# Kernel optimization log

Hardware: AMD Instinct MI355X
Metric: run time of the kernel (lower is better)

The kernel has to match this reference:

```python
import jax, jax.numpy as jnp
import numpy as np

N_NODES = 50000
N_EDGES = 800000
N_GRAPHS = 256
D_IN, D_H1, D_H2, D_OUT = 64, 64, 64, 64


def gcn_conv(x, W, b, src, dst, n_nodes):
    # PyG GCNConv (eval): h = x @ W; add self-loops; deg[i] = in_deg(i) + 1;
    # out[i] = sum_{j->i} h[j] * deg[i]^-1/2 deg[j]^-1/2 + h[i]/deg[i] + b
    h = x @ W  # [N, F]
    ones = jnp.ones((src.shape[0],), dtype=x.dtype)
    deg = jax.ops.segment_sum(ones, dst, num_segments=n_nodes) + 1.0  # self loop
    dinv = jax.lax.rsqrt(deg)
    norm = dinv[src] * dinv[dst]  # [E]
    msg = h[src] * norm[:, None]  # [E, F]  (memory-bound gather)
    agg = jax.ops.segment_sum(msg, dst, num_segments=n_nodes)  # scatter-add
    agg = agg + h * (1.0 / deg)[:, None]  # self-loop contribution
    return agg + b


def setup_inputs() -> dict:
    key = jax.random.key(0)
    ks = jax.random.split(key, 12)
    x = jax.random.normal(ks[0], (N_NODES, D_IN), dtype=jnp.float32)
    src = jax.random.randint(ks[1], (N_EDGES,), 0, N_NODES)
    dst = jax.random.randint(ks[2], (N_EDGES,), 0, N_NODES)
    batch = jnp.sort(jax.random.randint(ks[3], (N_NODES,), 0, N_GRAPHS))
    def glorot(k, fin, fout):
        s = jnp.sqrt(6.0 / (fin + fout))
        return jax.random.uniform(k, (fin, fout), jnp.float32, -s, s)
    return {
        "x": x, "src": src, "dst": dst, "batch": batch,
        "W1": glorot(ks[4], D_IN, D_H1), "b1": jnp.zeros((D_H1,), jnp.float32),
        "W2": glorot(ks[5], D_H1, D_H2), "b2": jnp.zeros((D_H2,), jnp.float32),
        "W3": glorot(ks[6], D_H2, D_OUT), "b3": jnp.zeros((D_OUT,), jnp.float32),
        "Wl": glorot(ks[7], D_OUT, 1), "bl": jnp.zeros((1,), jnp.float32),
    }


def reference(x, src, dst, batch, W1, b1, W2, b2, W3, b3, Wl, bl):
    n = x.shape[0]
    h = jax.nn.relu(gcn_conv(x, W1, b1, src, dst, n))   # dropout inactive (eval)
    h = jax.nn.relu(gcn_conv(h, W2, b2, src, dst, n))
    h = jax.nn.relu(gcn_conv(h, W3, b3, src, dst, n))
    # global_mean_pool over graph ids
    sums = jax.ops.segment_sum(h, batch, num_segments=N_GRAPHS)  # [G, F]
    cnt = jax.ops.segment_sum(jnp.ones((n,), h.dtype), batch, num_segments=N_GRAPHS)
    pooled = sums / jnp.maximum(cnt, 1.0)[:, None]
    return pooled @ Wl + bl  # [G, 1]
```

## Files before the change

kernel.cpp:

```cpp
#include <hip/hip_runtime.h>

#define N_NODES 50000
#define N_EDGES 800000
#define N_GRAPHS 256
#define F 64
#define NBUCK 196
#define CAP 4608
#define P3_TILE 2048
#define P3_GRID ((N_EDGES + P3_TILE - 1) / P3_TILE)
#define BCAP 6144

__device__ __forceinline__ unsigned short f2bf(float f) {
    union { float f; unsigned u; } c; c.f = f;
    unsigned u = c.u + 0x7FFFu + ((c.u >> 16) & 1u);
    return (unsigned short)(u >> 16);
}
__device__ __forceinline__ unsigned pack2bf(float lo, float hi) {
    return (unsigned)f2bf(lo) | ((unsigned)f2bf(hi) << 16);
}
__device__ __forceinline__ float bfl(unsigned u) {
    union { unsigned u; float f; } c; c.u = u << 16; return c.f;
}
__device__ __forceinline__ float bfh(unsigned u) {
    union { unsigned u; float f; } c; c.u = u & 0xFFFF0000u; return c.f;
}

__global__ __launch_bounds__(256) void partition_edges(const int* __restrict__ src,
                                                       const int* __restrict__ dst,
                                                       int* __restrict__ bcur,
                                                       unsigned int* __restrict__ bpair) {
    __shared__ int bh[NBUCK], bloc[NBUCK], bpos[NBUCK];
    int t = threadIdx.x;
    int lo = blockIdx.x * P3_TILE;
    int hi = min(lo + P3_TILE, N_EDGES);
    for (int i = t; i < NBUCK; i += 256) { bh[i] = 0; bpos[i] = 0; }
    __syncthreads();
    for (int e = lo + t; e < hi; e += 256) atomicAdd(&bh[dst[e] >> 8], 1);
    __syncthreads();
    for (int i = t; i < NBUCK; i += 256)
        bloc[i] = bh[i] ? atomicAdd(&bcur[i], bh[i]) : 0;
    __syncthreads();
    for (int e = lo + t; e < hi; e += 256) {
        int d = dst[e];
        int b = d >> 8;
        int r = atomicAdd(&bpos[b], 1);
        bpair[(size_t)b * CAP + bloc[b] + r] = ((unsigned)src[e] << 8) | (unsigned)(d & 255);
    }
}

__global__ __launch_bounds__(256) void bucket_sort(const unsigned int* __restrict__ bpair,
                                                   const int* __restrict__ bcur,
                                                   int* __restrict__ eidx,
                                                   int* __restrict__ rbeg,
                                                   int* __restrict__ rend,
                                                   float* __restrict__ dinv) {
    __shared__ int cnt[256], s[256], pos[256];
    __shared__ int lout[BCAP];
    int b = blockIdx.x, t = threadIdx.x;
    int base = b * CAP;
    int sz = bcur[b];

    cnt[t] = 0;
    __syncthreads();
    for (int i = t; i < sz; i += 256) atomicAdd(&cnt[bpair[base + i] & 255], 1);
    __syncthreads();
    int v = cnt[t];
    s[t] = v;
    __syncthreads();
    for (int off = 1; off < 256; off <<= 1) {
        int u = (t >= off) ? s[t - off] : 0;
        __syncthreads();
        s[t] += u;
        __syncthreads();
    }
    int excl = s[t] - v;
    pos[t] = excl;
    int node = b * 256 + t;
    if (node < N_NODES) {
        rbeg[node] = base + excl;
        rend[node] = base + excl + v;
        dinv[node] = 1.0f / sqrtf((float)v + 1.0f);
    }
    __syncthreads();

    if (sz <= BCAP) {
        for (int i = t; i < sz; i += 256) {
            unsigned p = bpair[base + i];
            int r = atomicAdd(&pos[p & 255], 1);
            lout[r] = (int)((p >> 8) << 7);
        }
        __syncthreads();
        for (int i = t; i < sz; i += 256) eidx[base + i] = lout[i];
    } else {
        for (int i = t; i < sz; i += 256) {
            unsigned p = bpair[base + i];
            int r = atomicAdd(&pos[p & 255], 1);
            eidx[base + r] = (int)((p >> 8) << 7);
        }
    }
}

#define XSTRIDE 17
template <bool BF16IN>
__global__ __launch_bounds__(256) void gemm64_t(const void* __restrict__ Xv,
                                                const float* __restrict__ W,
                                                const float* __restrict__ dinv,
                                                unsigned short* __restrict__ Hn, int n) {
    __shared__ float4 sW[64 * 16];
    __shared__ float4 sX[128 * XSTRIDE];
    int tid = threadIdx.x;
    int base = blockIdx.x * 128;

    const float4* W4 = (const float4*)W;
    for (int i = tid; i < 64 * 16; i += 256) sW[i] = W4[i];
    if (BF16IN) {
        const uint4* X4 = (const uint4*)Xv;
        for (int i = tid; i < 128 * 8; i += 256) {
            int r = i >> 3, c = i & 7;
            int node = base + r;
            uint4 u = (node < n) ? X4[(size_t)node * 8 + c]
                                 : make_uint4(0u, 0u, 0u, 0u);
            sX[r * XSTRIDE + 2 * c]     = make_float4(bfl(u.x), bfh(u.x), bfl(u.y), bfh(u.y));
            sX[r * XSTRIDE + 2 * c + 1] = make_float4(bfl(u.z), bfh(u.z), bfl(u.w), bfh(u.w));
        }
    } else {
        const float4* X4 = (const float4*)Xv;
        for (int i = tid; i < 128 * 16; i += 256) {
            int r = i >> 4, kg = i & 15;
            int node = base + r;
            sX[r * XSTRIDE + kg] = (node < n) ? X4[(size_t)node * 16 + kg]
                                              : make_float4(0.f, 0.f, 0.f, 0.f);
        }
    }
    __syncthreads();

    int fg = tid & 15;
    int ng = tid >> 4;
    float4 acc[8];
#pragma unroll
    for (int ii = 0; ii < 8; ii++) acc[ii] = make_float4(0.f, 0.f, 0.f, 0.f);

    for (int kg = 0; kg < 16; kg++) {
        float4 xv[8];
#pragma unroll
        for (int ii = 0; ii < 8; ii++) xv[ii] = sX[(ng + 16 * ii) * XSTRIDE + kg];
#pragma unroll
        for (int kk = 0; kk < 4; kk++) {
            float4 wv = sW[(4 * kg + kk) * 16 + fg];
#pragma unroll
            for (int ii = 0; ii < 8; ii++) {
                float xs = (kk == 0) ? xv[ii].x : (kk == 1) ? xv[ii].y
                         : (kk == 2) ? xv[ii].z : xv[ii].w;
                acc[ii].x += wv.x * xs;
                acc[ii].y += wv.y * xs;
                acc[ii].z += wv.z * xs;
                acc[ii].w += wv.w * xs;
            }
        }
    }

    ushort4* H4 = (ushort4*)Hn;
#pragma unroll
    for (int ii = 0; ii < 8; ii++) {
        int node = base + ng + 16 * ii;
        if (node < n) {
            float d = dinv[node];
            float4 o = acc[ii];
            ushort4 u;
            u.x = f2bf(o.x * d); u.y = f2bf(o.y * d);
            u.z = f2bf(o.z * d); u.w = f2bf(o.w * d);
            H4[(size_t)node * 16 + fg] = u;
        }
    }
}

__global__ __launch_bounds__(256) void gather_layer(const int* __restrict__ rbeg,
                                                    const int* __restrict__ rend,
                                                    const int* __restrict__ eidx,
                                                    const float* __restrict__ dinv,
                                                    const unsigned short* __restrict__ Hn,
                                                    const float* __restrict__ b,
                                                    unsigned short* __restrict__ OUT, int n) {
    int wv = (blockIdx.x * blockDim.x + threadIdx.x) >> 6;
    int lane = threadIdx.x & 63;
    int ns = lane >> 3, f = lane & 7;
    int node = wv * 8 + ns;
    bool valid = node < n;
    int beg = valid ? rbeg[node] : 0;
    int end = valid ? rend[node] : 0;
    const char* Hb = (const char*)Hn;

    float a0 = 0.f, a1 = 0.f, a2 = 0.f, a3 = 0.f;
    float a4 = 0.f, a5 = 0.f, a6 = 0.f, a7 = 0.f;
    int k = beg;
    for (; k + 1 < end; k += 2) {
        int o1 = eidx[k];
        int o2 = eidx[k + 1];
        uint4 p = *(const uint4*)(Hb + o1 + f * 16);
        uint4 q = *(const uint4*)(Hb + o2 + f * 16);
        a0 += bfl(p.x) + bfl(q.x); a1 += bfh(p.x) + bfh(q.x);
        a2 += bfl(p.y) + bfl(q.y); a3 += bfh(p.y) + bfh(q.y);
        a4 += bfl(p.z) + bfl(q.z); a5 += bfh(p.z) + bfh(q.z);
        a6 += bfl(p.w) + bfl(q.w); a7 += bfh(p.w) + bfh(q.w);
    }
    if (k < end) {
        int o1 = eidx[k];
        uint4 p = *(const uint4*)(Hb + o1 + f * 16);
        a0 += bfl(p.x); a1 += bfh(p.x);
        a2 += bfl(p.y); a3 += bfh(p.y);
        a4 += bfl(p.z); a5 += bfh(p.z);
        a6 += bfl(p.w); a7 += bfh(p.w);
    }

    if (valid) {
        float di = dinv[node];
        uint4 hs = *(const uint4*)(Hb + (size_t)node * 128 + f * 16);
        float4 b0 = ((const float4*)b)[2 * f];
        float4 b1 = ((const float4*)b)[2 * f + 1];
        float v0 = fmaxf(di * (a0 + bfl(hs.x)) + b0.x, 0.f);
        float v1 = fmaxf(di * (a1 + bfh(hs.x)) + b0.y, 0.f);
        float v2 = fmaxf(di * (a2 + bfl(hs.y)) + b0.z, 0.f);
        float v3 = fmaxf(di * (a3 + bfh(hs.y)) + b0.w, 0.f);
        float v4 = fmaxf(di * (a4 + bfl(hs.z)) + b1.x, 0.f);
        float v5 = fmaxf(di * (a5 + bfh(hs.z)) + b1.y, 0.f);
        float v6 = fmaxf(di * (a6 + bfl(hs.w)) + b1.z, 0.f);
        float v7 = fmaxf(di * (a7 + bfh(hs.w)) + b1.w, 0.f);
        uint4 u;
        u.x = pack2bf(v0, v1); u.y = pack2bf(v2, v3);
        u.z = pack2bf(v4, v5); u.w = pack2bf(v6, v7);
        ((uint4*)OUT)[(size_t)node * 8 + f] = u;
    }
}

__global__ __launch_bounds__(256) void gather_pool(const int* __restrict__ rbeg,
                                                   const int* __restrict__ rend,
                                                   const int* __restrict__ eidx,
                                                   const float* __restrict__ dinv,
                                                   const unsigned short* __restrict__ Hn,
                                                   const float* __restrict__ b,
                                                   const float* __restrict__ Wl,
                                                   float* __restrict__ pdot, int n) {
    int wv = (blockIdx.x * blockDim.x + threadIdx.x) >> 6;
    int lane = threadIdx.x & 63;
    int ns = lane >> 3, f = lane & 7;
    int node = wv * 8 + ns;
    bool valid = node < n;
    int beg = valid ? rbeg[node] : 0;
    int end = valid ? rend[node] : 0;
    const char* Hb = (const char*)Hn;

    float a0 = 0.f, a1 = 0.f, a2 = 0.f, a3 = 0.f;
    float a4 = 0.f, a5 = 0.f, a6 = 0.f, a7 = 0.f;
    int k = beg;
    for (; k + 1 < end; k += 2) {
        int o1 = eidx[k];
        int o2 = eidx[k + 1];
        uint4 p = *(const uint4*)(Hb + o1 + f * 16);
        uint4 q = *(const uint4*)(Hb + o2 + f * 16);
        a0 += bfl(p.x) + bfl(q.x); a1 += bfh(p.x) + bfh(q.x);
        a2 += bfl(p.y) + bfl(q.y); a3 += bfh(p.y) + bfh(q.y);
        a4 += bfl(p.z) + bfl(q.z); a5 += bfh(p.z) + bfh(q.z);
        a6 += bfl(p.w) + bfl(q.w); a7 += bfh(p.w) + bfh(q.w);
    }
    if (k < end) {
        int o1 = eidx[k];
        uint4 p = *(const uint4*)(Hb + o1 + f * 16);
        a0 += bfl(p.x); a1 += bfh(p.x);
        a2 += bfl(p.y); a3 += bfh(p.y);
        a4 += bfl(p.z); a5 += bfh(p.z);
        a6 += bfl(p.w); a7 += bfh(p.w);
    }

    float di = valid ? dinv[node] : 0.f;
    uint4 hs = valid ? *(const uint4*)(Hb + (size_t)node * 128 + f * 16)
                     : make_uint4(0u, 0u, 0u, 0u);
    float4 b0 = ((const float4*)b)[2 * f];
    float4 b1 = ((const float4*)b)[2 * f + 1];
    float4 w0 = ((const float4*)Wl)[2 * f];
    float4 w1 = ((const float4*)Wl)[2 * f + 1];
    float d = 0.f;
    d += fmaxf(di * (a0 + bfl(hs.x)) + b0.x, 0.f) * w0.x;
    d += fmaxf(di * (a1 + bfh(hs.x)) + b0.y, 0.f) * w0.y;
    d += fmaxf(di * (a2 + bfl(hs.y)) + b0.z, 0.f) * w0.z;
    d += fmaxf(di * (a3 + bfh(hs.y)) + b0.w, 0.f) * w0.w;
    d += fmaxf(di * (a4 + bfl(hs.z)) + b1.x, 0.f) * w1.x;
    d += fmaxf(di * (a5 + bfh(hs.z)) + b1.y, 0.f) * w1.y;
    d += fmaxf(di * (a6 + bfl(hs.w)) + b1.z, 0.f) * w1.z;
    d += fmaxf(di * (a7 + bfh(hs.w)) + b1.w, 0.f) * w1.w;
#pragma unroll
    for (int m = 1; m <= 4; m <<= 1) d += __shfl_xor(d, m);
    if (valid && f == 0) pdot[node] = d;
}

__global__ __launch_bounds__(64) void final_out(const float* __restrict__ pdot,
                                                const int* __restrict__ batch,
                                                const float* __restrict__ bl,
                                                float* __restrict__ out) {
    int g = blockIdx.x;
    __shared__ int slo, shi;
    int lane = threadIdx.x;
    if (lane == 0) {
        int a = 0, b = N_NODES;
        while (a < b) { int m = (a + b) >> 1; if (batch[m] < g) a = m + 1; else b = m; }
        slo = a;
        b = N_NODES;
        while (a < b) { int m = (a + b) >> 1; if (batch[m] < g + 1) a = m + 1; else b = m; }
        shi = a;
    }
    __syncthreads();
    int lo = slo, hi = shi;
    float acc = 0.f;
    for (int i = lo + lane; i < hi; i += 64) acc += pdot[i];
#pragma unroll
    for (int off = 32; off > 0; off >>= 1) acc += __shfl_down(acc, off);
    if (lane == 0) {
        float cnt = (float)(hi - lo);
        out[g] = acc / fmaxf(cnt, 1.0f) + bl[0];
    }
}

extern "C" void kernel_launch(void* const* d_in, const int* in_sizes, int n_in,
                              void* d_out, int out_size, void* d_ws, size_t ws_size,
                              hipStream_t stream) {
    const float* x     = (const float*)d_in[0];
    const int*   src   = (const int*)d_in[1];
    const int*   dst   = (const int*)d_in[2];
    const int*   batch = (const int*)d_in[3];
    const float* W1 = (const float*)d_in[4];  const float* b1 = (const float*)d_in[5];
    const float* W2 = (const float*)d_in[6];  const float* b2 = (const float*)d_in[7];
    const float* W3 = (const float*)d_in[8];  const float* b3 = (const float*)d_in[9];
    const float* Wl = (const float*)d_in[10]; const float* bl = (const float*)d_in[11];
    float* out = (float*)d_out;

    char* ws = (char*)d_ws;
    unsigned short* Abf = (unsigned short*)ws;
    unsigned short* Bbf = Abf + (size_t)N_NODES * F;
    float* dinv    = (float*)(Bbf + (size_t)N_NODES * F);
    float* pdot    = dinv + N_NODES;
    int*   rbeg    = (int*)(pdot + N_NODES);
    int*   rend    = rbeg + N_NODES;
    int*   bcur    = rend + N_NODES;
    unsigned int* bpair = (unsigned int*)(bcur + NBUCK);
    int*   eidx    = (int*)(bpair + (size_t)NBUCK * CAP);

    const int GEMM_GRID   = (N_NODES + 127) / 128;
    const int GATHER_GRID = (N_NODES + 31) / 32;

    hipMemsetAsync(bcur, 0, NBUCK * sizeof(int), stream);
    partition_edges<<<P3_GRID, 256, 0, stream>>>(src, dst, bcur, bpair);
    bucket_sort<<<NBUCK, 256, 0, stream>>>(bpair, bcur, eidx, rbeg, rend, dinv);

    gemm64_t<false><<<GEMM_GRID, 256, 0, stream>>>((const void*)x, W1, dinv, Abf, N_NODES);
    gather_layer<<<GATHER_GRID, 256, 0, stream>>>(rbeg, rend, eidx, dinv, Abf, b1, Bbf, N_NODES);

    gemm64_t<true><<<GEMM_GRID, 256, 0, stream>>>((const void*)Bbf, W2, dinv, Abf, N_NODES);
    gather_layer<<<GATHER_GRID, 256, 0, stream>>>(rbeg, rend, eidx, dinv, Abf, b2, Bbf, N_NODES);

    gemm64_t<true><<<GEMM_GRID, 256, 0, stream>>>((const void*)Bbf, W3, dinv, Abf, N_NODES);
    gather_pool<<<GATHER_GRID, 256, 0, stream>>>(rbeg, rend, eidx, dinv, Abf, b3, Wl, pdot, N_NODES);

    final_out<<<N_GRAPHS, 64, 0, stream>>>(pdot, batch, bl, out);
}
```

Baseline: 221.9 us.

## Reorder gather nodes by in-degree to balance per-wave work

Builds a degree histogram in bucket_sort, scans it, and scatters node ids into a permutation sorted by in-degree bin. The gather kernels then process nodes through this permutation, so the 8 nodes sharing a wave have similar edge counts and lanes idle less while waiting on the longest row. In exchange it adds two small kernels and an extra indirection, and output writes and the self-row load become scattered instead of contiguous.

```diff
diff --git a/kernel.cpp b/kernel.cpp
--- a/kernel.cpp
+++ b/kernel.cpp
@@ -9,6 +9,7 @@
 #define P3_TILE 2048
 #define P3_GRID ((N_EDGES + P3_TILE - 1) / P3_TILE)
 #define BCAP 6144
+#define DBINS 64
 
 __device__ __forceinline__ unsigned short f2bf(float f) {
     union { float f; unsigned u; } c; c.f = f;
@@ -53,14 +54,17 @@
                                                    int* __restrict__ eidx,
                                                    int* __restrict__ rbeg,
                                                    int* __restrict__ rend,
-                                                   float* __restrict__ dinv) {
+                                                   float* __restrict__ dinv,
+                                                   int* __restrict__ dhist) {
     __shared__ int cnt[256], s[256], pos[256];
     __shared__ int lout[BCAP];
+    __shared__ int ldh[DBINS];
     int b = blockIdx.x, t = threadIdx.x;
     int base = b * CAP;
     int sz = bcur[b];
 
     cnt[t] = 0;
+    if (t < DBINS) ldh[t] = 0;
     __syncthreads();
     for (int i = t; i < sz; i += 256) atomicAdd(&cnt[bpair[base + i] & 255], 1);
     __syncthreads();
@@ -80,8 +84,10 @@
         rbeg[node] = base + excl;
         rend[node] = base + excl + v;
         dinv[node] = 1.0f / sqrtf((float)v + 1.0f);
-    }
-    __syncthreads();
+        atomicAdd(&ldh[min(v, DBINS - 1)], 1);
+    }
+    __syncthreads();
+    if (t < DBINS && ldh[t]) atomicAdd(&dhist[t], ldh[t]);
 
     if (sz <= BCAP) {
         for (int i = t; i < sz; i += 256) {
@@ -97,6 +103,46 @@
             int r = atomicAdd(&pos[p & 255], 1);
             eidx[base + r] = (int)((p >> 8) << 7);
         }
+    }
+}
+
+__global__ __launch_bounds__(64) void dscan(const int* __restrict__ dhist,
+                                            int* __restrict__ dcur) {
+    __shared__ int s[DBINS];
+    int t = threadIdx.x;
+    int v = dhist[t];
+    s[t] = v;
+    __syncthreads();
+    for (int off = 1; off < DBINS; off <<= 1) {
+        int u = (t >= off) ? s[t - off] : 0;
+        __syncthreads();
+        s[t] += u;
+        __syncthreads();
+    }
+    dcur[t] = s[t] - v;
+}
+
+__global__ __launch_bounds__(256) void dscatter(const int* __restrict__ rbeg,
+                                                const int* __restrict__ rend,
+                                                int* __restrict__ dcur,
+                                                int* __restrict__ perm) {
+    __shared__ int lh[DBINS], lbase[DBINS], lpos[DBINS];
+    int t = threadIdx.x;
+    int node = blockIdx.x * 256 + t;
+    for (int i = t; i < DBINS; i += 256) { lh[i] = 0; lpos[i] = 0; }
+    __syncthreads();
+    int bin = 0;
+    bool valid = node < N_NODES;
+    if (valid) {
+        bin = min(rend[node] - rbeg[node], DBINS - 1);
+        atomicAdd(&lh[bin], 1);
+    }
+    __syncthreads();
+    if (t < DBINS) lbase[t] = lh[t] ? atomicAdd(&dcur[t], lh[t]) : 0;
+    __syncthreads();
+    if (valid) {
+        int r = atomicAdd(&lpos[bin], 1);
+        perm[lbase[bin] + r] = node;
     }
 }
 
@@ -174,7 +220,8 @@
     }
 }
 
-__global__ __launch_bounds__(256) void gather_layer(const int* __restrict__ rbeg,
+__global__ __launch_bounds__(256) void gather_layer(const int* __restrict__ perm,
+                                                    const int* __restrict__ rbeg,
                                                     const int* __restrict__ rend,
                                                     const int* __restrict__ eidx,
                                                     const float* __restrict__ dinv,
@@ -184,8 +231,9 @@
     int wv = (blockIdx.x * blockDim.x + threadIdx.x) >> 6;
     int lane = threadIdx.x & 63;
     int ns = lane >> 3, f = lane & 7;
-    int node = wv * 8 + ns;
-    bool valid = node < n;
+    int slot = wv * 8 + ns;
+    bool valid = slot < n;
+    int node = valid ? perm[slot] : 0;
     int beg = valid ? rbeg[node] : 0;
     int end = valid ? rend[node] : 0;
     const char* Hb = (const char*)Hn;
@@ -232,7 +280,8 @@
     }
 }
 
-__global__ __launch_bounds__(256) void gather_pool(const int* __restrict__ rbeg,
+__global__ __launch_bounds__(256) void gather_pool(const int* __restrict__ perm,
+                                                   const int* __restrict__ rbeg,
                                                    const int* __restrict__ rend,
                                                    const int* __restrict__ eidx,
                                                    const float* __restrict__ dinv,
@@ -243,8 +292,9 @@
     int wv = (blockIdx.x * blockDim.x + threadIdx.x) >> 6;
     int lane = threadIdx.x & 63;
     int ns = lane >> 3, f = lane & 7;
-    int node = wv * 8 + ns;
-    bool valid = node < n;
+    int slot = wv * 8 + ns;
+    bool valid = slot < n;
+    int node = valid ? perm[slot] : 0;
     int beg = valid ? rbeg[node] : 0;
     int end = valid ? rend[node] : 0;
     const char* Hb = (const char*)Hn;
@@ -339,25 +389,31 @@
     float* pdot    = dinv + N_NODES;
     int*   rbeg    = (int*)(pdot + N_NODES);
     int*   rend    = rbeg + N_NODES;
-    int*   bcur    = rend + N_NODES;
-    unsigned int* bpair = (unsigned int*)(bcur + NBUCK);
+    int*   perm    = rend + N_NODES;
+    int*   bcur    = perm + N_NODES;
+    int*   dhist   = bcur + NBUCK;
+    int*   dcur    = dhist + DBINS;
+    unsigned int* bpair = (unsigned int*)(dcur + DBINS);
     int*   eidx    = (int*)(bpair + (size_t)NBUCK * CAP);
 
     const int GEMM_GRID   = (N_NODES + 127) / 128;
     const int GATHER_GRID = (N_NODES + 31) / 32;
-
-    hipMemsetAsync(bcur, 0, NBUCK * sizeof(int), stream);
+    const int NODE_GRID   = (N_NODES + 255) / 256;
+
+    hipMemsetAsync(bcur, 0, (NBUCK + DBINS) * sizeof(int), stream);
     partition_edges<<<P3_GRID, 256, 0, stream>>>(src, dst, bcur, bpair);
-    bucket_sort<<<NBUCK, 256, 0, stream>>>(bpair, bcur, eidx, rbeg, rend, dinv);
+    bucket_sort<<<NBUCK, 256, 0, stream>>>(bpair, bcur, eidx, rbeg, rend, dinv, dhist);
+    dscan<<<1, DBINS, 0, stream>>>(dhist, dcur);
+    dscatter<<<NODE_GRID, 256, 0, stream>>>(rbeg, rend, dcur, perm);
 
     gemm64_t<false><<<GEMM_GRID, 256, 0, stream>>>((const void*)x, W1, dinv, Abf, N_NODES);
-    gather_layer<<<GATHER_GRID, 256, 0, stream>>>(rbeg, rend, eidx, dinv, Abf, b1, Bbf, N_NODES);
+    gather_layer<<<GATHER_GRID, 256, 0, stream>>>(perm, rbeg, rend, eidx, dinv, Abf, b1, Bbf, N_NODES);
 
     gemm64_t<true><<<GEMM_GRID, 256, 0, stream>>>((const void*)Bbf, W2, dinv, Abf, N_NODES);
-    gather_layer<<<GATHER_GRID, 256, 0, stream>>>(rbeg, rend, eidx, dinv, Abf, b2, Bbf, N_NODES);
+    gather_layer<<<GATHER_GRID, 256, 0, stream>>>(perm, rbeg, rend, eidx, dinv, Abf, b2, Bbf, N_NODES);
 
     gemm64_t<true><<<GEMM_GRID, 256, 0, stream>>>((const void*)Bbf, W3, dinv, Abf, N_NODES);
-    gather_pool<<<GATHER_GRID, 256, 0, stream>>>(rbeg, rend, eidx, dinv, Abf, b3, Wl, pdot, N_NODES);
+    gather_pool<<<GATHER_GRID, 256, 0, stream>>>(perm, rbeg, rend, eidx, dinv, Abf, b3, Wl, pdot, N_NODES);
 
     final_out<<<N_GRAPHS, 64, 0, stream>>>(pdot, batch, bl, out);
 }
```

New measurement: 236.3 us. +6.5%, slower.
